# Kernel tuning notes

Hardware: AMD Instinct MI355X
Metric: run time of the kernel (lower is better)

## Reference

```python
import jax, jax.numpy as jnp
import numpy as np

N, E, D_IN, D_OUT = 16384, 4096, 256, 256


def _leaky(v):
    return jnp.where(v > 0, v, 0.1 * v)


def setup_inputs() -> dict:
    key = jax.random.key(0)
    ks = jax.random.split(key, 8)
    x = jax.random.normal(ks[0], (N, D_IN), dtype=jnp.float32)
    # 0/1 incidence mask, float32 (as multiplied in the torch code)
    H_shape = jax.random.randint(ks[1], (N, E), 0, 2).astype(jnp.float32)
    w1 = jax.random.normal(ks[2], (D_IN, D_OUT), dtype=jnp.float32)
    w2 = jax.random.normal(ks[3], (D_OUT, D_OUT), dtype=jnp.float32)
    a1 = jax.random.normal(ks[4], (D_OUT, 1), dtype=jnp.float32)
    a21 = jax.random.normal(ks[5], (D_OUT, 1), dtype=jnp.float32)
    a22 = jax.random.normal(ks[6], (D_OUT, 1), dtype=jnp.float32)
    return {"x": x, "H_shape": H_shape, "w1": w1, "w2": w2,
            "a1": a1, "a21": a21, "a22": a22}


def reference(x, H_shape, w1, w2, a1, a21, a22):
    xw1 = x @ w1                                  # [N, D]
    # node->edge attention (masked softmax-like over nodes, axis -2)
    f = _leaky(xw1) @ a1                          # [N, 1]
    e = jnp.exp(jnp.tanh(f / 8) * 8) * H_shape    # [N, E]
    e = e / jnp.sum(e, axis=-2, keepdims=True)    # normalize over nodes
    # edge features
    f = _leaky(e.T @ xw1)                         # [E, D]
    # edge->node attention (masked normalize over edges, axis -1)
    b = (_leaky(f @ w2) @ a21).T + _leaky(xw1) @ a22  # [1,E] + [N,1] -> [N,E]
    b = jnp.exp(jnp.tanh(b / 8) * 8) * H_shape
    b = b / jnp.sum(b, axis=-1, keepdims=True)
    return _leaky(b @ f @ w2)                     # [N, D]
```

## Files before the change

### kernel.cpp

```cpp
#include <hip/hip_runtime.h>


typedef __attribute__((ext_vector_type(8))) short short8;
typedef __attribute__((ext_vector_type(4))) short short4v;
typedef __attribute__((ext_vector_type(4))) float f32x4;
typedef __attribute__((ext_vector_type(4))) int int4v;
typedef __attribute__((ext_vector_type(4))) unsigned int uint4v;

__device__ __forceinline__ float leakyf(float v) { return v > 0.f ? v : 0.1f * v; }
__device__ __forceinline__ float fastrcp(float x) { return __builtin_amdgcn_rcpf(x); }

__device__ __forceinline__ float satexpf(float t) {
    float u = fminf(fmaxf(t * 0.25f, -30.f), 30.f);
    float p = __expf(u);
    float th = (p - 1.f) * fastrcp(p + 1.f);
    return __expf(8.f * th);
}

__device__ __forceinline__ short f2b(float v) {
    unsigned int x = __float_as_uint(v);
    x += 0x7fffu + ((x >> 16) & 1u);
    return (short)(x >> 16);
}
__device__ __forceinline__ float b2f(short s) {
    return __uint_as_float(((unsigned int)(unsigned short)s) << 16);
}
__device__ __forceinline__ unsigned int bits4_to_bytes(unsigned int s) {
    return ((s & 0xFu) * 0x00204081u) & 0x01010101u;
}

__global__ __launch_bounds__(256) void transpose_split2(
        const float* __restrict__ s0, short* __restrict__ dh0, short* __restrict__ dl0,
        const float* __restrict__ s1, short* __restrict__ dh1, short* __restrict__ dl1) {
    const float* src = blockIdx.z ? s1 : s0;
    short* dh = blockIdx.z ? dh1 : dh0;
    short* dl = blockIdx.z ? dl1 : dl0;
    __shared__ float Ts[64][65];
    const int t = threadIdx.x;
    const long r0 = (long)blockIdx.x * 64;
    const long c0 = (long)blockIdx.y * 64;
    {
        const int row = t >> 2, cc = (t & 3) * 16;
        const float* p = src + (r0 + row) * 256 + c0 + cc;
#pragma unroll
        for (int i = 0; i < 4; ++i) {
            f32x4 v = *reinterpret_cast<const f32x4*>(p + i * 4);
#pragma unroll
            for (int k = 0; k < 4; ++k) Ts[row][cc + i * 4 + k] = v[k];
        }
    }
    __syncthreads();
    {
        const int cl = t >> 2, ch = (t & 3) * 16;
        short8 h0, h1, l0, l1;
#pragma unroll
        for (int i = 0; i < 8; ++i) {
            float v = Ts[ch + i][cl];
            short h = f2b(v);
            h0[i] = h; l0[i] = f2b(v - b2f(h));
        }
#pragma unroll
        for (int i = 0; i < 8; ++i) {
            float v = Ts[ch + 8 + i][cl];
            short h = f2b(v);
            h1[i] = h; l1[i] = f2b(v - b2f(h));
        }
        short* qh = dh + (c0 + cl) * 256 + r0 + ch;
        short* ql = dl + (c0 + cl) * 256 + r0 + ch;
        *reinterpret_cast<short8*>(qh) = h0;
        *reinterpret_cast<short8*>(qh + 8) = h1;
        *reinterpret_cast<short8*>(ql) = l0;
        *reinterpret_cast<short8*>(ql + 8) = l1;
    }
}

__global__ __launch_bounds__(256) void transposeH_pack(
        const float* __restrict__ H, unsigned int* __restrict__ Hbits,
        unsigned int* __restrict__ HbitsT, unsigned int* __restrict__ ddmax,
        float* __restrict__ cat) {
    __shared__ float Ts[64][65];
    const int t = threadIdx.x;
    const long r0 = (long)blockIdx.x * 64;
    const long c0 = (long)blockIdx.y * 64;
    if (blockIdx.x == 0 && blockIdx.y == 0) {
        if (t < 256) ddmax[t] = 0u;
        if (t < 32) ddmax[256 + t] = 0u;
#pragma unroll
        for (int i = 0; i < 16; ++i) cat[t * 16 + i] = 0.f;
    }
    {
        const int row = t >> 2, cc = (t & 3) * 16;
        const float* p = H + (r0 + row) * 4096L + c0 + cc;
#pragma unroll
        for (int i = 0; i < 4; ++i) {
            f32x4 v = *reinterpret_cast<const f32x4*>(p + i * 4);
#pragma unroll
            for (int k = 0; k < 4; ++k) Ts[row][cc + i * 4 + k] = v[k];
        }
    }
    __syncthreads();
    if (t < 128) {
        const int nl = t >> 1, w = t & 1;
        unsigned int u = 0;
#pragma unroll
        for (int b = 0; b < 32; ++b)
            u |= (Ts[nl][w * 32 + b] != 0.f ? 1u : 0u) << b;
        Hbits[(r0 + nl) * 128 + (c0 >> 5) + w] = u;
    } else {
        const int t2 = t - 128;
        const int jl = t2 >> 1, w = t2 & 1;
        unsigned int u = 0;
#pragma unroll
        for (int b = 0; b < 32; ++b)
            u |= (Ts[w * 32 + b][jl] != 0.f ? 1u : 0u) << b;
        HbitsT[(c0 + jl) * 512 + (r0 >> 5) + w] = u;
    }
}

__global__ __launch_bounds__(256) void gemm_xw1(
        const float* __restrict__ A, const short* __restrict__ Bh,
        const short* __restrict__ Bl, float* __restrict__ C) {
    __shared__ short Ash[128][72];
    __shared__ short Asl[128][72];
    __shared__ short Bsh[64][72];
    __shared__ short Bsl[64][72];
    const int t = threadIdx.x;
    const int wid = t >> 6, lane = t & 63;
    const int wm = wid & 1, wn = wid >> 1;
    const int quad = lane >> 4, l15 = lane & 15;
    const long m0 = (long)blockIdx.x * 128;
    const long n0 = (long)blockIdx.y * 64;
    f32x4 acc[4][2];
#pragma unroll
    for (int i = 0; i < 4; ++i)
#pragma unroll
        for (int j = 0; j < 2; ++j)
#pragma unroll
            for (int r = 0; r < 4; ++r) acc[i][j][r] = 0.f;

    for (int kb = 0; kb < 256; kb += 64) {
#pragma unroll
        for (int it = 0; it < 4; ++it) {
            const int cid = t + it * 256;
            const int row = cid >> 3, c8 = (cid & 7) * 8;
            const float* ap = A + (m0 + row) * 256 + kb + c8;
            f32x4 v0 = *reinterpret_cast<const f32x4*>(ap);
            f32x4 v1 = *reinterpret_cast<const f32x4*>(ap + 4);
            short8 hi, lo;
#pragma unroll
            for (int k = 0; k < 4; ++k) {
                short h0 = f2b(v0[k]); hi[k] = h0; lo[k] = f2b(v0[k] - b2f(h0));
                short h1 = f2b(v1[k]); hi[4 + k] = h1; lo[4 + k] = f2b(v1[k] - b2f(h1));
            }
            *reinterpret_cast<short8*>(&Ash[row][c8]) = hi;
            *reinterpret_cast<short8*>(&Asl[row][c8]) = lo;
        }
#pragma unroll
        for (int it = 0; it < 2; ++it) {
            const int cid = t + it * 256;
            const int row = cid >> 3, c8 = (cid & 7) * 8;
            *reinterpret_cast<short8*>(&Bsh[row][c8]) =
                *reinterpret_cast<const short8*>(Bh + (n0 + row) * 256 + kb + c8);
            *reinterpret_cast<short8*>(&Bsl[row][c8]) =
                *reinterpret_cast<const short8*>(Bl + (n0 + row) * 256 + kb + c8);
        }
        __syncthreads();
#pragma unroll
        for (int ks = 0; ks < 2; ++ks) {
            short8 ah[4], al[4], bh[2], bl[2];
#pragma unroll
            for (int i = 0; i < 4; ++i) {
                ah[i] = *reinterpret_cast<const short8*>(&Ash[wm * 64 + i * 16 + l15][ks * 32 + quad * 8]);
                al[i] = *reinterpret_cast<const short8*>(&Asl[wm * 64 + i * 16 + l15][ks * 32 + quad * 8]);
            }
#pragma unroll
            for (int j = 0; j < 2; ++j) {
                bh[j] = *reinterpret_cast<const short8*>(&Bsh[wn * 32 + j * 16 + l15][ks * 32 + quad * 8]);
                bl[j] = *reinterpret_cast<const short8*>(&Bsl[wn * 32 + j * 16 + l15][ks * 32 + quad * 8]);
            }
#pragma unroll
            for (int i = 0; i < 4; ++i)
#pragma unroll
                for (int j = 0; j < 2; ++j) {
                    acc[i][j] = __builtin_amdgcn_mfma_f32_16x16x32_bf16(ah[i], bh[j], acc[i][j], 0, 0, 0);
                    acc[i][j] = __builtin_amdgcn_mfma_f32_16x16x32_bf16(ah[i], bl[j], acc[i][j], 0, 0, 0);
                    acc[i][j] = __builtin_amdgcn_mfma_f32_16x16x32_bf16(al[i], bh[j], acc[i][j], 0, 0, 0);
                }
        }
        __syncthreads();
    }
#pragma unroll
    for (int i = 0; i < 4; ++i) {
        const long grow = m0 + wm * 64 + i * 16 + quad * 4;
#pragma unroll
        for (int j = 0; j < 2; ++j) {
            const long gcol = n0 + wn * 32 + j * 16 + l15;
#pragma unroll
            for (int r = 0; r < 4; ++r)
                C[(grow + r) * 256 + gcol] = acc[i][j][r];
        }
    }
}

__global__ __launch_bounds__(256) void node_stats1(
        const float* __restrict__ xw1, const float* __restrict__ a1,
        const float* __restrict__ a22, float* __restrict__ g_out,
        float* __restrict__ dn, unsigned int* __restrict__ ddmax) {
    __shared__ float Mx[4][260];
    const int t = threadIdx.x;
    const int n0 = blockIdx.x * 64;
    const int r = t >> 2, q = t & 3;
    const long n = n0 + r;
    const float* xp = xw1 + n * 256 + q * 64;
    float vals[64];
    float facc = 0.f, dacc = 0.f;
#pragma unroll
    for (int i = 0; i < 16; ++i) {
        f32x4 v  = *reinterpret_cast<const f32x4*>(xp + i * 4);
        f32x4 b1 = *reinterpret_cast<const f32x4*>(a1 + q * 64 + i * 4);
        f32x4 b2 = *reinterpret_cast<const f32x4*>(a22 + q * 64 + i * 4);
#pragma unroll
        for (int k = 0; k < 4; ++k) {
            float lv = leakyf(v[k]);
            facc += lv * b1[k];
            dacc += lv * b2[k];
            vals[i * 4 + k] = v[k];
        }
    }
    facc += __shfl_xor(facc, 1); facc += __shfl_xor(facc, 2);
    dacc += __shfl_xor(dacc, 1); dacc += __shfl_xor(dacc, 2);
    const float g = satexpf(facc);
    if (q == 0) { dn[n] = dacc; g_out[n] = g; }
    float lm[64];
#pragma unroll
    for (int i = 0; i < 64; ++i) lm[i] = fabsf(vals[i] * g);
#pragma unroll
    for (int m = 4; m < 64; m <<= 1)
#pragma unroll
        for (int i = 0; i < 64; ++i) lm[i] = fmaxf(lm[i], __shfl_xor(lm[i], m));
    float gm = g;
#pragma unroll
    for (int m = 1; m < 64; m <<= 1) gm = fmaxf(gm, __shfl_xor(gm, m));
    const int wv = t >> 6, lane = t & 63;
    if (lane < 4) {
#pragma unroll
        for (int i = 0; i < 64; ++i) Mx[wv][lane * 64 + i] = lm[i];
    }
    if (lane == 0) Mx[wv][256] = gm;
    __syncthreads();
    if (t < 256) {
        float m = fmaxf(fmaxf(Mx[0][t], Mx[1][t]), fmaxf(Mx[2][t], Mx[3][t]));
        atomicMax(&ddmax[t], __float_as_uint(m));
    }
    if (t == 0) {
        float m = fmaxf(fmaxf(Mx[0][256], Mx[1][256]), fmaxf(Mx[2][256], Mx[3][256]));
        atomicMax(&ddmax[256], __float_as_uint(m));
    }
}

__global__ __launch_bounds__(256) void quantize_y(
        const float* __restrict__ xw1, const float* __restrict__ g_in,
        const unsigned int* __restrict__ ddmax, char* __restrict__ yQ) {
    __shared__ unsigned int Qh[257][16];
    __shared__ unsigned int Ql[257][16];
    const int t = threadIdx.x;
    const int n0 = blockIdx.x * 64;
    const int dd0 = (t >> 4) * 16;
    const int w = t & 15;
    const int r4 = w * 4;
    float s[16];
#pragma unroll
    for (int i = 0; i < 16; ++i)
        s[i] = 32512.f / __uint_as_float(ddmax[dd0 + i]);
    const float sg = 32512.f / __uint_as_float(ddmax[256]);
    unsigned int bh[16], bl[16];
#pragma unroll
    for (int i = 0; i < 16; ++i) { bh[i] = 0u; bl[i] = 0u; }
    unsigned int gh = 0u, gl = 0u;
#pragma unroll
    for (int rr = 0; rr < 4; ++rr) {
        const long n = n0 + r4 + rr;
        const float gg = g_in[n];
        const float* xp = xw1 + n * 256 + dd0;
#pragma unroll
        for (int c = 0; c < 4; ++c) {
            f32x4 v = *reinterpret_cast<const f32x4*>(xp + c * 4);
#pragma unroll
            for (int k = 0; k < 4; ++k) {
                const int i = c * 4 + k;
                int qv = __float2int_rn(v[k] * gg * s[i]);
                qv = max(-32639, min(32639, qv));
                const int qh = (qv + 128) >> 8;
                const int ql = qv - (qh << 8);
                bh[i] |= ((unsigned int)(qh & 255)) << (8 * rr);
                bl[i] |= ((unsigned int)(ql & 255)) << (8 * rr);
            }
        }
        if (t < 16) {
            int qv = __float2int_rn(gg * sg);
            qv = max(-32639, min(32639, qv));
            const int qh = (qv + 128) >> 8;
            const int ql = qv - (qh << 8);
            gh |= ((unsigned int)(qh & 255)) << (8 * rr);
            gl |= ((unsigned int)(ql & 255)) << (8 * rr);
        }
    }
#pragma unroll
    for (int i = 0; i < 16; ++i) { Qh[dd0 + i][w] = bh[i]; Ql[dd0 + i][w] = bl[i]; }
    if (t < 16) { Qh[256][t] = gh; Ql[256][t] = gl; }
    __syncthreads();
#pragma unroll
    for (int it = 0; it < 2; ++it) {
        const int dd = it * 256 + t;
        if (dd < 288) {
#pragma unroll
            for (int s2 = 0; s2 < 4; ++s2) {
                uint4v vh, vl;
                if (dd < 257) {
                    vh = *reinterpret_cast<const uint4v*>(&Qh[dd][s2 * 4]);
                    vl = *reinterpret_cast<const uint4v*>(&Ql[dd][s2 * 4]);
                } else {
#pragma unroll
                    for (int k = 0; k < 4; ++k) { vh[k] = 0u; vl[k] = 0u; }
                }
                *reinterpret_cast<uint4v*>(yQ + (long)dd * 16384 + n0 + s2 * 16) = vh;
                *reinterpret_cast<uint4v*>(yQ + (long)(288 + dd) * 16384 + n0 + s2 * 16) = vl;
            }
        }
    }
}

__global__ __launch_bounds__(256) void gemm_c1_bits(
        const unsigned int* __restrict__ HbitsT, const char* __restrict__ Bb,
        float* __restrict__ Cp) {
    __shared__ char Bsh[48][144];
    __shared__ char Bsl[48][144];
    const int t = threadIdx.x;
    const int wid = t >> 6, lane = t & 63;
    const int quad = lane >> 4, l15 = lane & 15;
    const long m0 = (long)blockIdx.x * 256;
    const long n0 = (long)blockIdx.y * 48;
    const long k0 = (long)blockIdx.z * 2048;
    float* Cz = Cp + (long)blockIdx.z * (4096L * 288);
    const unsigned int* bp[4];
#pragma unroll
    for (int i = 0; i < 4; ++i)
        bp[i] = HbitsT + (m0 + wid * 64 + i * 16 + l15) * 512 + (k0 >> 5);
    char* dstp[3];
    long sbase[3];
#pragma unroll
    for (int it = 0; it < 3; ++it) {
        const int cid = t + it * 256;
        const int idx = (cid < 384) ? cid : cid - 384;
        const int row = idx >> 3, seg = (idx & 7) * 16;
        dstp[it] = (cid >= 384) ? &Bsl[row][seg] : &Bsh[row][seg];
        const long srow = (cid >= 384) ? (288 + n0 + row) : (n0 + row);
        sbase[it] = srow * 16384 + k0 + seg;
    }
    int4v acch[4][3], accl[4][3];
#pragma unroll
    for (int i = 0; i < 4; ++i)
#pragma unroll
        for (int j = 0; j < 3; ++j)
#pragma unroll
            for (int r = 0; r < 4; ++r) { acch[i][j][r] = 0; accl[i][j][r] = 0; }

    uint4v bv[4], sv[3];
#pragma unroll
    for (int i = 0; i < 4; ++i)
        bv[i] = *reinterpret_cast<const uint4v*>(bp[i]);
#pragma unroll
    for (int it = 0; it < 3; ++it)
        sv[it] = *reinterpret_cast<const uint4v*>(Bb + sbase[it]);

    for (int kb = 0; kb < 2048; kb += 128) {
#pragma unroll
        for (int it = 0; it < 3; ++it)
            *reinterpret_cast<uint4v*>(dstp[it]) = sv[it];
        __syncthreads();
        const bool pf = (kb < 1920);
        uint4v bvn[4], svn[3];
        if (pf) {
#pragma unroll
            for (int i = 0; i < 4; ++i)
                bvn[i] = *reinterpret_cast<const uint4v*>(bp[i] + ((kb + 128) >> 5));
#pragma unroll
            for (int it = 0; it < 3; ++it)
                svn[it] = *reinterpret_cast<const uint4v*>(Bb + sbase[it] + kb + 128);
        }
#pragma unroll
        for (int ks = 0; ks < 2; ++ks) {
            int4v af[4], bh[3], bl[3];
#pragma unroll
            for (int i = 0; i < 4; ++i) {
                const unsigned int u =
                    bv[i][ks * 2 + (quad >> 1)] >> ((quad & 1) * 16);
                uint4v e;
#pragma unroll
                for (int k = 0; k < 4; ++k) e[k] = bits4_to_bytes(u >> (4 * k));
                af[i] = __builtin_bit_cast(int4v, e);
            }
#pragma unroll
            for (int j = 0; j < 3; ++j) {
                bh[j] = *reinterpret_cast<const int4v*>(&Bsh[j * 16 + l15][ks * 64 + quad * 16]);
                bl[j] = *reinterpret_cast<const int4v*>(&Bsl[j * 16 + l15][ks * 64 + quad * 16]);
            }
#pragma unroll
            for (int i = 0; i < 4; ++i)
#pragma unroll
                for (int j = 0; j < 3; ++j) {
                    acch[i][j] = __builtin_amdgcn_mfma_i32_16x16x64_i8(af[i], bh[j], acch[i][j], 0, 0, 0);
                    accl[i][j] = __builtin_amdgcn_mfma_i32_16x16x64_i8(af[i], bl[j], accl[i][j], 0, 0, 0);
                }
        }
        __syncthreads();
        if (pf) {
#pragma unroll
            for (int i = 0; i < 4; ++i) bv[i] = bvn[i];
#pragma unroll
            for (int it = 0; it < 3; ++it) sv[it] = svn[it];
        }
    }
#pragma unroll
    for (int i = 0; i < 4; ++i) {
        const long grow = m0 + wid * 64 + i * 16 + quad * 4;
#pragma unroll
        for (int j = 0; j < 3; ++j) {
            const long gcol = n0 + j * 16 + l15;
#pragma unroll
            for (int r = 0; r < 4; ++r)
                Cz[(grow + r) * 288 + gcol] =
                    256.f * (float)acch[i][j][r] + (float)accl[i][j][r];
        }
    }
}

__global__ __launch_bounds__(256) void reduce_C1(
        const float* __restrict__ C1p, const unsigned int* __restrict__ ddmax,
        float* __restrict__ C1) {
    const int i = blockIdx.x * 256 + threadIdx.x;
    const int dd = i % 288;
    float s = 0.f;
#pragma unroll
    for (int z = 0; z < 8; ++z) s += C1p[(long)z * 4096 * 288 + i];
    C1[i] = s * (__uint_as_float(ddmax[dd]) * (1.f / 32512.f));
}

__global__ __launch_bounds__(256) void gemm_G(
        const float* __restrict__ C1, const short* __restrict__ w2Th,
        const short* __restrict__ w2Tl, const float* __restrict__ a21,
        short* __restrict__ GT, float* __restrict__ cat) {
    __shared__ short Ash[64][72];
    __shared__ short Asl[64][72];
    __shared__ short Bsh[64][72];
    __shared__ short Bsl[64][72];
    __shared__ float Gs[64][65];
    const int t = threadIdx.x;
    const int wid = t >> 6, lane = t & 63;
    const int wm = wid & 1, wn = wid >> 1;
    const int quad = lane >> 4, l15 = lane & 15;
    const long j0 = (long)blockIdx.x * 64;
    const long d0 = (long)blockIdx.y * 64;
    f32x4 acc[2][2];
#pragma unroll
    for (int i = 0; i < 2; ++i)
#pragma unroll
        for (int j = 0; j < 2; ++j)
#pragma unroll
            for (int r = 0; r < 4; ++r) acc[i][j][r] = 0.f;

    for (int kb = 0; kb < 256; kb += 64) {
#pragma unroll
        for (int it = 0; it < 2; ++it) {
            const int cid = t + it * 256;
            const int row = cid >> 3, c8 = (cid & 7) * 8;
            const float rd = fastrcp(C1[(j0 + row) * 288 + 256]);
            const float* ap = C1 + (j0 + row) * 288 + kb + c8;
            f32x4 v0 = *reinterpret_cast<const f32x4*>(ap);
            f32x4 v1 = *reinterpret_cast<const f32x4*>(ap + 4);
            short8 hi, lo;
#pragma unroll
            for (int k = 0; k < 4; ++k) {
                float f0 = leakyf(v0[k] * rd);
                float f1 = leakyf(v1[k] * rd);
                short h0 = f2b(f0); hi[k] = h0; lo[k] = f2b(f0 - b2f(h0));
                short h1 = f2b(f1); hi[4 + k] = h1; lo[4 + k] = f2b(f1 - b2f(h1));
            }
            *reinterpret_cast<short8*>(&Ash[row][c8]) = hi;
            *reinterpret_cast<short8*>(&Asl[row][c8]) = lo;
            *reinterpret_cast<short8*>(&Bsh[row][c8]) =
                *reinterpret_cast<const short8*>(w2Th + (d0 + row) * 256 + kb + c8);
            *reinterpret_cast<short8*>(&Bsl[row][c8]) =
                *reinterpret_cast<const short8*>(w2Tl + (d0 + row) * 256 + kb + c8);
        }
        __syncthreads();
#pragma unroll
        for (int ks = 0; ks < 2; ++ks) {
            short8 ah[2], al[2], bh[2], bl[2];
#pragma unroll
            for (int i = 0; i < 2; ++i) {
                ah[i] = *reinterpret_cast<const short8*>(&Ash[wm * 32 + i * 16 + l15][ks * 32 + quad * 8]);
                al[i] = *reinterpret_cast<const short8*>(&Asl[wm * 32 + i * 16 + l15][ks * 32 + quad * 8]);
            }
#pragma unroll
            for (int j = 0; j < 2; ++j) {
                bh[j] = *reinterpret_cast<const short8*>(&Bsh[wn * 32 + j * 16 + l15][ks * 32 + quad * 8]);
                bl[j] = *reinterpret_cast<const short8*>(&Bsl[wn * 32 + j * 16 + l15][ks * 32 + quad * 8]);
            }
#pragma unroll
            for (int i = 0; i < 2; ++i)
#pragma unroll
                for (int j = 0; j < 2; ++j) {
                    acc[i][j] = __builtin_amdgcn_mfma_f32_16x16x32_bf16(ah[i], bh[j], acc[i][j], 0, 0, 0);
                    acc[i][j] = __builtin_amdgcn_mfma_f32_16x16x32_bf16(ah[i], bl[j], acc[i][j], 0, 0, 0);
                    acc[i][j] = __builtin_amdgcn_mfma_f32_16x16x32_bf16(al[i], bh[j], acc[i][j], 0, 0, 0);
                }
        }
        __syncthreads();
    }
#pragma unroll
    for (int i = 0; i < 2; ++i)
#pragma unroll
        for (int j = 0; j < 2; ++j)
#pragma unroll
            for (int r = 0; r < 4; ++r)
                Gs[wm * 32 + i * 16 + quad * 4 + r][wn * 32 + j * 16 + l15] = acc[i][j][r];
    __syncthreads();
    {
        const int jl = t >> 2, q = t & 3;
        float cp = 0.f;
#pragma unroll
        for (int i = 0; i < 16; ++i) {
            const int d = q * 16 + i;
            cp += leakyf(Gs[jl][d]) * a21[d0 + d];
        }
        cp += __shfl_xor(cp, 1); cp += __shfl_xor(cp, 2);
        if (q == 0) atomicAdd(&cat[j0 + jl], cp);
    }
    {
        const int dl = t >> 2, q = t & 3;
        short8 pk0, pk1;
#pragma unroll
        for (int i = 0; i < 8; ++i) pk0[i] = f2b(Gs[q * 16 + i][dl]);
#pragma unroll
        for (int i = 0; i < 8; ++i) pk1[i] = f2b(Gs[q * 16 + 8 + i][dl]);
        short* gp = GT + (d0 + dl) * 4096 + j0 + q * 16;
        *reinterpret_cast<short8*>(gp) = pk0;
        *reinterpret_cast<short8*>(gp + 8) = pk1;
    }
}

__global__ __launch_bounds__(512, 4) void fused_out_split(
        const unsigned int* __restrict__ Hbits, const float* __restrict__ cat,
        const float* __restrict__ dn, const short* __restrict__ GT,
        float* __restrict__ outP, float* __restrict__ rsP) {
    __shared__ short As[64][72];
    __shared__ short Bs[256][72];
    __shared__ float rsS[64][8];
    const int t = threadIdx.x;
    const int wid = t >> 6, lane = t & 63;
    const int wm = wid >> 2, wn = wid & 3;
    const int quad = lane >> 4, l15 = lane & 15;
    const long m0 = (long)blockIdx.x * 64;
    const int z = blockIdx.y;
    const int kbase = z * 1024;
    const int r = t & 63, c8 = t >> 6;
    const float drow = dn[m0 + r];
    const int bo = (c8 & 3) * 8;

    f32x4 acc[2][4];
#pragma unroll
    for (int i = 0; i < 2; ++i)
#pragma unroll
        for (int j = 0; j < 4; ++j)
#pragma unroll
            for (int x = 0; x < 4; ++x) acc[i][j][x] = 0.f;
    float racc = 0.f;

    short8 gv[4];
    short8 pkc;
    {
        const int kb = kbase;
#pragma unroll
        for (int it = 0; it < 4; ++it) {
            const int cid = t + it * 512;
            const int row = cid >> 3, cc = (cid & 7) * 8;
            gv[it] = *reinterpret_cast<const short8*>(GT + row * 4096 + kb + cc);
        }
        const unsigned int w = Hbits[(m0 + r) * 128 + (kb >> 5) + (c8 >> 2)];
        const f32x4 cv0 = *reinterpret_cast<const f32x4*>(cat + kb + c8 * 8);
        const f32x4 cv1 = *reinterpret_cast<const f32x4*>(cat + kb + c8 * 8 + 4);
#pragma unroll
        for (int k = 0; k < 8; ++k) {
            const float cvk = (k < 4) ? cv0[k & 3] : cv1[k & 3];
            const float s = ((w >> (bo + k)) & 1u) ? satexpf(cvk + drow) : 0.f;
            const short sb = f2b(s);
            pkc[k] = sb;
            racc += b2f(sb);
        }
    }

    for (int kk = 0; kk < 1024; kk += 64) {
#pragma unroll
        for (int it = 0; it < 4; ++it) {
            const int cid = t + it * 512;
            const int row = cid >> 3, cc = (cid & 7) * 8;
            *reinterpret_cast<short8*>(&Bs[row][cc]) = gv[it];
        }
        *reinterpret_cast<short8*>(&As[r][c8 * 8]) = pkc;
        __syncthreads();

        const bool pf = (kk < 960);
        unsigned int hw = 0u;
        f32x4 cn0{}, cn1{};
        if (pf) {
            const int kn = kbase + kk + 64;
#pragma unroll
            for (int it = 0; it < 4; ++it) {
                const int cid = t + it * 512;
                const int row = cid >> 3, cc = (cid & 7) * 8;
                gv[it] = *reinterpret_cast<const short8*>(GT + row * 4096 + kn + cc);
            }
            hw = Hbits[(m0 + r) * 128 + (kn >> 5) + (c8 >> 2)];
            cn0 = *reinterpret_cast<const f32x4*>(cat + kn + c8 * 8);
            cn1 = *reinterpret_cast<const f32x4*>(cat + kn + c8 * 8 + 4);
        }

#pragma unroll
        for (int ks = 0; ks < 2; ++ks) {
            short8 af[2], bf[4];
#pragma unroll
            for (int i = 0; i < 2; ++i)
                af[i] = *reinterpret_cast<const short8*>(
                        &As[wm * 32 + i * 16 + l15][ks * 32 + quad * 8]);
#pragma unroll
            for (int j = 0; j < 4; ++j)
                bf[j] = *reinterpret_cast<const short8*>(
                        &Bs[wn * 64 + j * 16 + l15][ks * 32 + quad * 8]);
#pragma unroll
            for (int i = 0; i < 2; ++i)
#pragma unroll
                for (int j = 0; j < 4; ++j)
                    acc[i][j] = __builtin_amdgcn_mfma_f32_16x16x32_bf16(
                            af[i], bf[j], acc[i][j], 0, 0, 0);
        }

        if (pf) {
#pragma unroll
            for (int k = 0; k < 8; ++k) {
                const float cvk = (k < 4) ? cn0[k & 3] : cn1[k & 3];
                const float s = ((hw >> (bo + k)) & 1u) ? satexpf(cvk + drow) : 0.f;
                const short sb = f2b(s);
                pkc[k] = sb;
                racc += b2f(sb);
            }
        }
        __syncthreads();
    }
    rsS[r][c8] = racc;
    __syncthreads();
    if (t < 64) {
        float s = 0.f;
#pragma unroll
        for (int i = 0; i < 8; ++i) s += rsS[t][i];
        rsP[z * 16384 + m0 + t] = s;
    }
    float* op = outP + (long)z * (16384L * 256);
#pragma unroll
    for (int i = 0; i < 2; ++i) {
#pragma unroll
        for (int j = 0; j < 4; ++j) {
            const long gcol = wn * 64 + j * 16 + l15;
#pragma unroll
            for (int x = 0; x < 4; ++x) {
                const long grow = m0 + wm * 32 + i * 16 + quad * 4 + x;
                op[grow * 256 + gcol] = acc[i][j][x];
            }
        }
    }
}

__global__ __launch_bounds__(256) void combine_out(
        const float* __restrict__ outP, const float* __restrict__ rsP,
        float* __restrict__ out) {
    const long i = ((long)blockIdx.x * 256 + threadIdx.x) * 4;
    const long n = i >> 8;
    f32x4 s = *reinterpret_cast<const f32x4*>(outP + i);
#pragma unroll
    for (int z = 1; z < 4; ++z) {
        f32x4 v = *reinterpret_cast<const f32x4*>(outP + (long)z * (16384L * 256) + i);
#pragma unroll
        for (int k = 0; k < 4; ++k) s[k] += v[k];
    }
    const float rinv = fastrcp(rsP[n] + rsP[16384 + n] + rsP[32768 + n] + rsP[49152 + n]);
    f32x4 o;
#pragma unroll
    for (int k = 0; k < 4; ++k) o[k] = leakyf(s[k] * rinv);
    *reinterpret_cast<f32x4*>(out + i) = o;
}

extern "C" void kernel_launch(void* const* d_in, const int* in_sizes, int n_in,
                              void* d_out, int out_size, void* d_ws, size_t ws_size,
                              hipStream_t stream) {
    const float* x   = (const float*)d_in[0];
    const float* H   = (const float*)d_in[1];
    const float* w1  = (const float*)d_in[2];
    const float* w2  = (const float*)d_in[3];
    const float* a1  = (const float*)d_in[4];
    const float* a21 = (const float*)d_in[5];
    const float* a22 = (const float*)d_in[6];
    float* out = (float*)d_out;
    char* ws = (char*)d_ws;

    float* xw1   = (float*)(ws + 0);
    float* C1p   = (float*)(ws + 0);
    char*  yQ    = (char*)(ws + 67108864);
    float* dn    = (float*)(ws + 76546048);
    float* g     = (float*)(ws + 76611584);
    unsigned int* ddmax = (unsigned int*)(ws + 76677120);
    short* w1Th  = (short*)(ws + 76681216);
    short* w1Tl  = (short*)(ws + 76812288);
    short* w2Th  = (short*)(ws + 76943360);
    short* w2Tl  = (short*)(ws + 77074432);
    float* C1    = (float*)(ws + 77205504);
    short* GT    = (short*)(ws + 81924096);
    float* cat   = (float*)(ws + 84021248);
    unsigned int* Hbits  = (unsigned int*)(ws + 84037632);
    unsigned int* HbitsT = (unsigned int*)(ws + 92426240);
    float* outP  = (float*)(ws + 134217728);
    float* rsP   = (float*)(ws + 201326592);

    transpose_split2<<<dim3(4, 4, 2), 256, 0, stream>>>(
            w1, w1Th, w1Tl, w2, w2Th, w2Tl);
    transposeH_pack<<<dim3(256, 64), 256, 0, stream>>>(H, Hbits, HbitsT, ddmax, cat);

    gemm_xw1<<<dim3(128, 4), 256, 0, stream>>>(x, w1Th, w1Tl, xw1);
    node_stats1<<<dim3(256), 256, 0, stream>>>(xw1, a1, a22, g, dn, ddmax);
    quantize_y<<<dim3(256), 256, 0, stream>>>(xw1, g, ddmax, yQ);

    gemm_c1_bits<<<dim3(16, 6, 8), 256, 0, stream>>>(HbitsT, yQ, C1p);
    reduce_C1<<<dim3(4608), 256, 0, stream>>>(C1p, ddmax, C1);

    gemm_G<<<dim3(64, 4), 256, 0, stream>>>(C1, w2Th, w2Tl, a21, GT, cat);

    fused_out_split<<<dim3(256, 4), 512, 0, stream>>>(Hbits, cat, dn, GT, outP, rsP);
    combine_out<<<dim3(4096), 256, 0, stream>>>(outP, rsP, out);
}
```

Before: 598.9 us.

## Drop split-K in final output GEMM and fuse normalization epilogue

Removes the 4-way split over the edge dimension in the final attention-weighted GEMM, so each block loops over all 4096 edges and applies the row-sum reciprocal and leaky activation directly in its epilogue. This eliminates the partial-output buffers (4x N×256 floats written and re-read) and the separate combine kernel launch. The trade-off is a grid of only 256 blocks instead of 1024, which may underfill the 256-CU device and lengthen each block's serial K loop.

```diff
diff --git a/kernel.cpp b/kernel.cpp
--- a/kernel.cpp
+++ b/kernel.cpp
@@ -550,20 +550,19 @@
     }
 }
 
-__global__ __launch_bounds__(512, 4) void fused_out_split(
+__global__ __launch_bounds__(512, 4) void fused_out(
         const unsigned int* __restrict__ Hbits, const float* __restrict__ cat,
         const float* __restrict__ dn, const short* __restrict__ GT,
-        float* __restrict__ outP, float* __restrict__ rsP) {
+        float* __restrict__ out) {
     __shared__ short As[64][72];
     __shared__ short Bs[256][72];
     __shared__ float rsS[64][8];
+    __shared__ float rs[64];
     const int t = threadIdx.x;
     const int wid = t >> 6, lane = t & 63;
     const int wm = wid >> 2, wn = wid & 3;
     const int quad = lane >> 4, l15 = lane & 15;
     const long m0 = (long)blockIdx.x * 64;
-    const int z = blockIdx.y;
-    const int kbase = z * 1024;
     const int r = t & 63, c8 = t >> 6;
     const float drow = dn[m0 + r];
     const int bo = (c8 & 3) * 8;
@@ -580,16 +579,15 @@
     short8 gv[4];
     short8 pkc;
     {
-        const int kb = kbase;
 #pragma unroll
         for (int it = 0; it < 4; ++it) {
             const int cid = t + it * 512;
             const int row = cid >> 3, cc = (cid & 7) * 8;
-            gv[it] = *reinterpret_cast<const short8*>(GT + row * 4096 + kb + cc);
-        }
-        const unsigned int w = Hbits[(m0 + r) * 128 + (kb >> 5) + (c8 >> 2)];
-        const f32x4 cv0 = *reinterpret_cast<const f32x4*>(cat + kb + c8 * 8);
-        const f32x4 cv1 = *reinterpret_cast<const f32x4*>(cat + kb + c8 * 8 + 4);
+            gv[it] = *reinterpret_cast<const short8*>(GT + row * 4096 + cc);
+        }
+        const unsigned int w = Hbits[(m0 + r) * 128 + (c8 >> 2)];
+        const f32x4 cv0 = *reinterpret_cast<const f32x4*>(cat + c8 * 8);
+        const f32x4 cv1 = *reinterpret_cast<const f32x4*>(cat + c8 * 8 + 4);
 #pragma unroll
         for (int k = 0; k < 8; ++k) {
             const float cvk = (k < 4) ? cv0[k & 3] : cv1[k & 3];
@@ -600,7 +598,7 @@
         }
     }
 
-    for (int kk = 0; kk < 1024; kk += 64) {
+    for (int kk = 0; kk < 4096; kk += 64) {
 #pragma unroll
         for (int it = 0; it < 4; ++it) {
             const int cid = t + it * 512;
@@ -610,11 +608,11 @@
         *reinterpret_cast<short8*>(&As[r][c8 * 8]) = pkc;
         __syncthreads();
 
-        const bool pf = (kk < 960);
+        const bool pf = (kk < 4032);
         unsigned int hw = 0u;
         f32x4 cn0{}, cn1{};
         if (pf) {
-            const int kn = kbase + kk + 64;
+            const int kn = kk + 64;
 #pragma unroll
             for (int it = 0; it < 4; ++it) {
                 const int cid = t + it * 512;
@@ -663,9 +661,9 @@
         float s = 0.f;
 #pragma unroll
         for (int i = 0; i < 8; ++i) s += rsS[t][i];
-        rsP[z * 16384 + m0 + t] = s;
-    }
-    float* op = outP + (long)z * (16384L * 256);
+        rs[t] = fastrcp(s);
+    }
+    __syncthreads();
 #pragma unroll
     for (int i = 0; i < 2; ++i) {
 #pragma unroll
@@ -673,30 +671,11 @@
             const long gcol = wn * 64 + j * 16 + l15;
 #pragma unroll
             for (int x = 0; x < 4; ++x) {
-                const long grow = m0 + wm * 32 + i * 16 + quad * 4 + x;
-                op[grow * 256 + gcol] = acc[i][j][x];
-            }
-        }
-    }
-}
-
-__global__ __launch_bounds__(256) void combine_out(
-        const float* __restrict__ outP, const float* __restrict__ rsP,
-        float* __restrict__ out) {
-    const long i = ((long)blockIdx.x * 256 + threadIdx.x) * 4;
-    const long n = i >> 8;
-    f32x4 s = *reinterpret_cast<const f32x4*>(outP + i);
-#pragma unroll
-    for (int z = 1; z < 4; ++z) {
-        f32x4 v = *reinterpret_cast<const f32x4*>(outP + (long)z * (16384L * 256) + i);
-#pragma unroll
-        for (int k = 0; k < 4; ++k) s[k] += v[k];
-    }
-    const float rinv = fastrcp(rsP[n] + rsP[16384 + n] + rsP[32768 + n] + rsP[49152 + n]);
-    f32x4 o;
-#pragma unroll
-    for (int k = 0; k < 4; ++k) o[k] = leakyf(s[k] * rinv);
-    *reinterpret_cast<f32x4*>(out + i) = o;
+                const int lrow = wm * 32 + i * 16 + quad * 4 + x;
+                out[(m0 + lrow) * 256 + gcol] = leakyf(acc[i][j][x] * rs[lrow]);
+            }
+        }
+    }
 }
 
 extern "C" void kernel_launch(void* const* d_in, const int* in_sizes, int n_in,
@@ -727,8 +706,6 @@
     float* cat   = (float*)(ws + 84021248);
     unsigned int* Hbits  = (unsigned int*)(ws + 84037632);
     unsigned int* HbitsT = (unsigned int*)(ws + 92426240);
-    float* outP  = (float*)(ws + 134217728);
-    float* rsP   = (float*)(ws + 201326592);
 
     transpose_split2<<<dim3(4, 4, 2), 256, 0, stream>>>(
             w1, w1Th, w1Tl, w2, w2Th, w2Tl);
@@ -743,6 +720,5 @@
 
     gemm_G<<<dim3(64, 4), 256, 0, stream>>>(C1, w2Th, w2Tl, a21, GT, cat);
 
-    fused_out_split<<<dim3(256, 4), 512, 0, stream>>>(Hbits, cat, dn, GT, outP, rsP);
-    combine_out<<<dim3(4096), 256, 0, stream>>>(outP, rsP, out);
-}
+    fused_out<<<dim3(256), 512, 0, stream>>>(Hbits, cat, dn, GT, out);
+}
```

Result: slower. 625.5 us (+4.4%).
